# Kernel tuning notes

Measured on AMD Instinct MI355X. Metric: run time of the kernel, lower is better.

The kernel has to match this reference:

```python
import jax, jax.numpy as jnp
import numpy as np

N = 250000   # num nodes
E = 250000   # num edges (tree: ~one parent per node)
D = 128      # embed_size
H = 256      # MLP hidden
HOPS = 3


def _mlp(x, w1, b1, w2, b2):
    # Sequential(Linear, ReLU, Linear, ReLU, Dropout(eval=identity))
    return jax.nn.relu(jnp.dot(jax.nn.relu(jnp.dot(x, w1) + b1), w2) + b2)


def _scatter_mean(src, idx, n):
    s = jax.ops.segment_sum(src, idx, num_segments=n)
    c = jax.ops.segment_sum(jnp.ones((src.shape[0],), src.dtype), idx, num_segments=n)
    return s / jnp.maximum(c, 1.0)[:, None]


def setup_inputs() -> dict:
    key = jax.random.key(0)
    ks = jax.random.split(key, 32)
    u = lambda k, shp: jax.random.uniform(k, shp, jnp.float32, -0.1, 0.1)
    inp = {
        "batch_token": jax.random.normal(ks[0], (N, D), jnp.float32),
        "self_idx_batch": jax.random.randint(ks[1], (E,), 0, N),
        "parent_idx_batch": jax.random.randint(ks[2], (E,), 0, N),
        "root_mask": (jax.random.uniform(ks[3], (N,)) < 0.01).astype(jnp.float32),
        "leaf_mask": (jax.random.uniform(ks[4], (N,)) < 0.3).astype(jnp.float32),
        "start_token": jax.random.normal(ks[5], (D,), jnp.float32),
        "end_token": jax.random.normal(ks[6], (D,), jnp.float32),
        # MLP_V: D -> H -> D
        "Vw1": u(ks[7], (D, H)), "Vb1": u(ks[8], (H,)), "Vw2": u(ks[9], (H, D)), "Vb2": u(ks[10], (D,)),
        # MLP_E: 1 -> H -> D
        "Ew1": u(ks[11], (1, H)), "Eb1": u(ks[12], (H,)), "Ew2": u(ks[13], (H, D)), "Eb2": u(ks[14], (D,)),
        # MLP_p: 3D -> H -> D
        "Pw1": u(ks[15], (3 * D, H)), "Pb1": u(ks[16], (H,)), "Pw2": u(ks[17], (H, D)), "Pb2": u(ks[18], (D,)),
        # MLP_c: 3D -> H -> D
        "Cw1": u(ks[19], (3 * D, H)), "Cb1": u(ks[20], (H,)), "Cw2": u(ks[21], (H, D)), "Cb2": u(ks[22], (D,)),
        # MLP_aggr: 3D -> H -> D
        "Aw1": u(ks[23], (3 * D, H)), "Ab1": u(ks[24], (H,)), "Aw2": u(ks[25], (H, D)), "Ab2": u(ks[26], (D,)),
    }
    return inp


def reference(batch_token, self_idx_batch, parent_idx_batch, root_mask, leaf_mask,
              start_token, end_token,
              Vw1, Vb1, Vw2, Vb2,
              Ew1, Eb1, Ew2, Eb2,
              Pw1, Pb1, Pw2, Pb2,
              Cw1, Cb1, Cw2, Cb2,
              Aw1, Ab1, Aw2, Ab2):
    n = batch_token.shape[0]
    edge_in = _mlp(jnp.ones((1, 1), batch_token.dtype), Ew1, Eb1, Ew2, Eb2)   # [1,D]
    edge_out = _mlp(jnp.zeros((1, 1), batch_token.dtype), Ew1, Eb1, Ew2, Eb2)  # [1,D]
    e = self_idx_batch.shape[0]
    edge_in = jnp.broadcast_to(edge_in, (e, edge_in.shape[1]))
    edge_out = jnp.broadcast_to(edge_out, (e, edge_out.shape[1]))

    hidden = _mlp(batch_token, Vw1, Vb1, Vw2, Vb2)  # [N,D]
    for _ in range(HOPS):
        node_self = hidden[self_idx_batch]      # [E,D] gather
        node_parent = hidden[parent_idx_batch]  # [E,D] gather
        inp_parent = jnp.concatenate([node_parent, node_self, edge_out], axis=-1)  # [E,3D]
        inp_child = jnp.concatenate([node_self, node_parent, edge_in], axis=-1)    # [E,3D]
        S_p = _mlp(inp_parent, Pw1, Pb1, Pw2, Pb2)
        S_c = _mlp(inp_child, Cw1, Cb1, Cw2, Cb2)
        S_p = _scatter_mean(S_p, self_idx_batch, n)
        S_c = _scatter_mean(S_c, parent_idx_batch, n)
        S_p = S_p + root_mask[:, None] * start_token
        S_c = S_c + leaf_mask[:, None] * end_token
        x_aggr = jnp.concatenate([hidden, S_p, S_c], axis=-1)  # [N,3D]
        hidden = hidden + _mlp(x_aggr, Aw1, Ab1, Aw2, Ab2)
    return hidden
```

## Files before the change

### kernel.cpp

```cpp
#include <hip/hip_runtime.h>

typedef __attribute__((ext_vector_type(8))) short short8;
typedef __attribute__((ext_vector_type(4))) float f32x4;

#define DD 128
#define HH 256

__device__ __forceinline__ unsigned short f2bf(float f) {
  unsigned int u = __float_as_uint(f);
  u += 0x7fffu + ((u >> 16) & 1u);
  return (unsigned short)(u >> 16);
}
__device__ __forceinline__ float bf2f(unsigned short s) {
  return __uint_as_float(((unsigned int)s) << 16);
}
__device__ __forceinline__ f32x4 mfma16(short8 a, short8 b, f32x4 c) {
  return __builtin_amdgcn_mfma_f32_16x16x32_bf16(a, b, c, 0, 0, 0);
}

__global__ void wconv_all(const float* __restrict__ s0, const float* __restrict__ s1,
                          const float* __restrict__ s2, const float* __restrict__ s3,
                          const float* __restrict__ s4, const float* __restrict__ s5,
                          const float* __restrict__ s6, const float* __restrict__ s7,
                          unsigned short* __restrict__ d0, unsigned short* __restrict__ d1,
                          unsigned short* __restrict__ d2, unsigned short* __restrict__ d3,
                          unsigned short* __restrict__ d4, unsigned short* __restrict__ d5,
                          unsigned short* __restrict__ d6, unsigned short* __restrict__ d7) {
  int id = blockIdx.x * 256 + threadIdx.x;
  const float* src; unsigned short* dst; int K, Nout, kswap = 0, base;
  if (id < 32768)       { src = s0; dst = d0; K = 128; Nout = 256; base = 0; }
  else if (id < 65536)  { src = s1; dst = d1; K = 256; Nout = 128; base = 32768; }
  else if (id < 131072) { src = s2; dst = d2; K = 256; Nout = 256; base = 65536; kswap = 128; }
  else if (id < 163840) { src = s3; dst = d3; K = 256; Nout = 128; base = 131072; }
  else if (id < 229376) { src = s4; dst = d4; K = 256; Nout = 256; base = 163840; }
  else if (id < 262144) { src = s5; dst = d5; K = 256; Nout = 128; base = 229376; }
  else if (id < 360448) { src = s6; dst = d6; K = 384; Nout = 256; base = 262144; }
  else if (id < 393216) { src = s7; dst = d7; K = 256; Nout = 128; base = 360448; }
  else return;
  int lid = id - base;
  int n = lid / K, k = lid - n * K;
  int ks = k + kswap; if (ks >= K) ks -= K;
  dst[n * K + k] = f2bf(src[(size_t)ks * Nout + n]);
}

__global__ void prep_bias(const float* __restrict__ Ew1, const float* __restrict__ Eb1,
                          const float* __restrict__ Ew2, const float* __restrict__ Eb2,
                          const float* __restrict__ Pw1, const float* __restrict__ Pb1,
                          const float* __restrict__ Cw1, const float* __restrict__ Cb1,
                          float* __restrict__ b1P, float* __restrict__ b1C) {
  __shared__ float h1[HH], h0[HH], ein[DD], eout[DD];
  int t = threadIdx.x;
  h1[t] = fmaxf(Ew1[t] + Eb1[t], 0.f);
  h0[t] = fmaxf(Eb1[t], 0.f);
  __syncthreads();
  if (t < DD) {
    float s1 = Eb2[t], s0 = Eb2[t];
    for (int j = 0; j < HH; ++j) { s1 += h1[j] * Ew2[j * DD + t]; s0 += h0[j] * Ew2[j * DD + t]; }
    ein[t]  = fmaxf(s1, 0.f);
    eout[t] = fmaxf(s0, 0.f);
  }
  __syncthreads();
  float bp = Pb1[t], bc = Cb1[t];
  for (int d = 0; d < DD; ++d) {
    bp += eout[d] * Pw1[(size_t)(256 + d) * HH + t];
    bc += ein[d]  * Cw1[(size_t)(256 + d) * HH + t];
  }
  b1P[t] = bp; b1C[t] = bc;
}

__global__ void count_k(const int* __restrict__ selfI, const int* __restrict__ parI,
                        int* degP, int* degC, int E) {
  int id = blockIdx.x * 256 + threadIdx.x;
  if (id < E) { atomicAdd(&degP[selfI[id]], 1); atomicAdd(&degC[parI[id]], 1); }
}

__global__ void scan1_2(const int* __restrict__ srcA, int* __restrict__ dstA, int* __restrict__ partA,
                        const int* __restrict__ srcB, int* __restrict__ dstB, int* __restrict__ partB,
                        int n) {
  const int* src = blockIdx.y ? srcB : srcA;
  int* dst = blockIdx.y ? dstB : dstA;
  int* part = blockIdx.y ? partB : partA;
  __shared__ int sh[256];
  int t = threadIdx.x;
  int base = blockIdx.x * 1024 + t * 4;
  int v0 = base + 0 < n ? src[base + 0] : 0;
  int v1 = base + 1 < n ? src[base + 1] : 0;
  int v2 = base + 2 < n ? src[base + 2] : 0;
  int v3 = base + 3 < n ? src[base + 3] : 0;
  int tsum = v0 + v1 + v2 + v3;
  sh[t] = tsum;
  __syncthreads();
  for (int off = 1; off < 256; off <<= 1) {
    int y = (t >= off) ? sh[t - off] : 0;
    __syncthreads();
    if (t >= off) sh[t] += y;
    __syncthreads();
  }
  int ex = sh[t] - tsum;
  if (base + 0 < n) dst[base + 0] = ex;
  if (base + 1 < n) dst[base + 1] = ex + v0;
  if (base + 2 < n) dst[base + 2] = ex + v0 + v1;
  if (base + 3 < n) dst[base + 3] = ex + v0 + v1 + v2;
  if (t == 255) part[blockIdx.x] = sh[255];
}

__global__ void scan2_2(int* __restrict__ partA, int* __restrict__ partB, int m) {
  int* part = blockIdx.x ? partB : partA;
  __shared__ int sh[256];
  int t = threadIdx.x;
  int carry = 0;
  for (int base = 0; base < m; base += 256) {
    int v = (base + t < m) ? part[base + t] : 0;
    sh[t] = v;
    __syncthreads();
    for (int off = 1; off < 256; off <<= 1) {
      int y = (t >= off) ? sh[t - off] : 0;
      __syncthreads();
      if (t >= off) sh[t] += y;
      __syncthreads();
    }
    if (base + t < m) part[base + t] = carry + sh[t] - v;
    int tot = sh[255];
    __syncthreads();
    carry += tot;
  }
}

__global__ void scan3copy(int* __restrict__ offP, const int* __restrict__ partA, int* __restrict__ curP,
                          int* __restrict__ offC, const int* __restrict__ partB, int* __restrict__ curC,
                          int n) {
  int i = blockIdx.x * 256 + threadIdx.x;
  if (i < n) {
    int a = offP[i] + partA[i >> 10];
    int b = offC[i] + partB[i >> 10];
    offP[i] = a; curP[i] = a;
    offC[i] = b; curC[i] = b;
  }
}

__global__ void pos_k(const int* __restrict__ selfI, const int* __restrict__ parI,
                      int* curP, int* curC, int* posP, int* posC, int E) {
  int e = blockIdx.x * 256 + threadIdx.x;
  if (e < E) {
    posP[e] = atomicAdd(&curP[selfI[e]], 1);
    posC[e] = atomicAdd(&curC[parI[e]], 1);
  }
}

__global__ void reorder_k(const int* __restrict__ selfI, const int* __restrict__ parI,
                          const int* __restrict__ posP, const int* __restrict__ posC,
                          int* __restrict__ selfS, int* __restrict__ parS,
                          int* __restrict__ posCS, int E) {
  int e = blockIdx.x * 256 + threadIdx.x;
  if (e < E) {
    int slot = posP[e];
    selfS[slot] = selfI[e];
    parS[slot] = parI[e];
    posCS[slot] = posC[e];
  }
}

__global__ __launch_bounds__(512, 4) void v_kernel(
    const float* __restrict__ x, const unsigned short* __restrict__ W1t,
    const unsigned short* __restrict__ W2t, const float* __restrict__ b1,
    const float* __restrict__ b2, float* __restrict__ hidden,
    unsigned short* __restrict__ hbf, int n) {
  __shared__ __align__(16) unsigned short A[64 * 136];
  __shared__ __align__(16) unsigned short O1[64 * 264];
  int t = threadIdx.x;
  int w = t >> 6, lane = t & 63, ln = lane & 15, quad = lane >> 4, qo = quad * 8;
  long tile0 = (long)blockIdx.x * 64;
  int rl = t >> 3, part = t & 7;
  int c0 = part * 16;
  long gr = tile0 + rl;
  const float* src = x + (size_t)(gr < n ? gr : 0) * DD + c0;
  unsigned short* arow = A + rl * 136 + c0;
#pragma unroll
  for (int i = 0; i < 4; ++i) {
    float4 v = *(const float4*)(src + i * 4);
    *(ushort4*)(arow + i * 4) = make_ushort4(f2bf(v.x), f2bf(v.y), f2bf(v.z), f2bf(v.w));
  }
  __syncthreads();
  f32x4 acc[4][2];
#pragma unroll
  for (int m = 0; m < 4; ++m) {
    acc[m][0] = {0.f, 0.f, 0.f, 0.f}; acc[m][1] = {0.f, 0.f, 0.f, 0.f};
  }
#pragma unroll
  for (int kt = 0; kt < 4; ++kt) {
    short8 a[4];
#pragma unroll
    for (int m = 0; m < 4; ++m)
      a[m] = *(const short8*)(A + (m * 16 + ln) * 136 + kt * 32 + qo);
#pragma unroll
    for (int nn = 0; nn < 2; ++nn) {
      short8 b = *(const short8*)(W1t + (size_t)(w * 32 + nn * 16 + ln) * 128 + kt * 32 + qo);
#pragma unroll
      for (int m = 0; m < 4; ++m) acc[m][nn] = mfma16(a[m], b, acc[m][nn]);
    }
  }
#pragma unroll
  for (int nn = 0; nn < 2; ++nn) {
    int col = w * 32 + nn * 16 + ln;
    float bb = b1[col];
#pragma unroll
    for (int m = 0; m < 4; ++m)
#pragma unroll
      for (int r = 0; r < 4; ++r)
        O1[(m * 16 + quad * 4 + r) * 264 + col] = f2bf(fmaxf(acc[m][nn][r] + bb, 0.f));
  }
  __syncthreads();
  f32x4 acc2[4];
#pragma unroll
  for (int m = 0; m < 4; ++m) acc2[m] = {0.f, 0.f, 0.f, 0.f};
#pragma unroll
  for (int kt = 0; kt < 8; ++kt) {
    short8 b = *(const short8*)(W2t + (size_t)(w * 16 + ln) * 256 + kt * 32 + qo);
#pragma unroll
    for (int m = 0; m < 4; ++m) {
      short8 a = *(const short8*)(O1 + (m * 16 + ln) * 264 + kt * 32 + qo);
      acc2[m] = mfma16(a, b, acc2[m]);
    }
  }
  {
    int col = w * 16 + ln;
    float bb = b2[col];
#pragma unroll
    for (int m = 0; m < 4; ++m)
#pragma unroll
      for (int r = 0; r < 4; ++r) {
        long gr2 = tile0 + m * 16 + quad * 4 + r;
        if (gr2 < n) {
          float v = fmaxf(acc2[m][r] + bb, 0.f);
          hidden[gr2 * DD + col] = v;
          if (hbf) hbf[gr2 * DD + col] = f2bf(v);
        }
      }
  }
}

__global__ __launch_bounds__(512, 4) void edge_kernel(
    const float* __restrict__ hidden, const unsigned short* __restrict__ hbf,
    const int* __restrict__ selfS, const int* __restrict__ parS,
    const int* __restrict__ posCS,
    const unsigned short* __restrict__ Pw1t, const unsigned short* __restrict__ Pw2t,
    const unsigned short* __restrict__ Cw1t, const unsigned short* __restrict__ Cw2t,
    const float* __restrict__ b1P, const float* __restrict__ b1C,
    const float* __restrict__ b2P, const float* __restrict__ b2C,
    unsigned short* __restrict__ SpE, unsigned short* __restrict__ ScE, int E) {
  __shared__ __align__(16) unsigned short A[64 * 264];
  __shared__ __align__(16) unsigned short O1[64 * 264];
  int t = threadIdx.x;
  int w = t >> 6, lane = t & 63, ln = lane & 15, quad = lane >> 4, qo = quad * 8;
  long tile0 = (long)blockIdx.x * 64;
  int rl = t >> 3, part = t & 7;
  long ge = tile0 + rl;
  bool vrow = ge < E;
  int si = vrow ? selfS[ge] : 0;
  int pi = vrow ? parS[ge] : 0;
  unsigned short* dstA = A + rl * 264 + part * 32;
  if (hbf) {
    const unsigned short* srcb = (part < 4) ? (hbf + (size_t)si * DD + part * 32)
                                            : (hbf + (size_t)pi * DD + (part - 4) * 32);
#pragma unroll
    for (int i = 0; i < 4; ++i)
      *(short8*)(dstA + i * 8) = *(const short8*)(srcb + i * 8);
  } else {
    const float* src = (part < 4) ? (hidden + (size_t)si * DD + part * 32)
                                  : (hidden + (size_t)pi * DD + (part - 4) * 32);
#pragma unroll
    for (int i = 0; i < 8; ++i) {
      float4 v = *(const float4*)(src + i * 4);
      *(ushort4*)(dstA + i * 4) = make_ushort4(f2bf(v.x), f2bf(v.y), f2bf(v.z), f2bf(v.w));
    }
  }
  __syncthreads();

  f32x4 accP[4][2], accC[4][2];
#pragma unroll
  for (int m = 0; m < 4; ++m) {
    accP[m][0] = {0.f, 0.f, 0.f, 0.f}; accP[m][1] = {0.f, 0.f, 0.f, 0.f};
    accC[m][0] = {0.f, 0.f, 0.f, 0.f}; accC[m][1] = {0.f, 0.f, 0.f, 0.f};
  }
#pragma unroll
  for (int kt = 0; kt < 8; ++kt) {
    short8 a[4];
#pragma unroll
    for (int m = 0; m < 4; ++m)
      a[m] = *(const short8*)(A + (m * 16 + ln) * 264 + kt * 32 + qo);
#pragma unroll
    for (int nn = 0; nn < 2; ++nn) {
      short8 bp = *(const short8*)(Pw1t + (size_t)(w * 32 + nn * 16 + ln) * 256 + kt * 32 + qo);
      short8 bc = *(const short8*)(Cw1t + (size_t)(w * 32 + nn * 16 + ln) * 256 + kt * 32 + qo);
#pragma unroll
      for (int m = 0; m < 4; ++m) {
        accP[m][nn] = mfma16(a[m], bp, accP[m][nn]);
        accC[m][nn] = mfma16(a[m], bc, accC[m][nn]);
      }
    }
  }

#pragma unroll
  for (int mlp = 0; mlp < 2; ++mlp) {
    const unsigned short* W2t = mlp ? Cw2t : Pw2t;
    const float* b1 = mlp ? b1C : b1P;
    const float* b2 = mlp ? b2C : b2P;
    unsigned short* Sout = mlp ? ScE : SpE;
#pragma unroll
    for (int nn = 0; nn < 2; ++nn) {
      int col = w * 32 + nn * 16 + ln;
      float bb = b1[col];
#pragma unroll
      for (int m = 0; m < 4; ++m)
#pragma unroll
        for (int r = 0; r < 4; ++r) {
          float v = mlp ? accC[m][nn][r] : accP[m][nn][r];
          O1[(m * 16 + quad * 4 + r) * 264 + col] = f2bf(fmaxf(v + bb, 0.f));
        }
    }
    __syncthreads();
    f32x4 acc2[4];
#pragma unroll
    for (int m = 0; m < 4; ++m) acc2[m] = {0.f, 0.f, 0.f, 0.f};
#pragma unroll
    for (int kt = 0; kt < 8; ++kt) {
      short8 b = *(const short8*)(W2t + (size_t)(w * 16 + ln) * 256 + kt * 32 + qo);
#pragma unroll
      for (int m = 0; m < 4; ++m) {
        short8 a = *(const short8*)(O1 + (m * 16 + ln) * 264 + kt * 32 + qo);
        acc2[m] = mfma16(a, b, acc2[m]);
      }
    }
    __syncthreads();
    {
      int col = w * 16 + ln;
      float bb = b2[col];
#pragma unroll
      for (int m = 0; m < 4; ++m)
#pragma unroll
        for (int r = 0; r < 4; ++r)
          O1[(m * 16 + quad * 4 + r) * 264 + col] = f2bf(fmaxf(acc2[m][r] + bb, 0.f));
    }
    __syncthreads();
    if (vrow) {
      size_t dpos = mlp ? (size_t)posCS[ge] : (size_t)ge;
      const unsigned short* srow = O1 + rl * 264 + part * 16;
      ushort4* dst = (ushort4*)(Sout + dpos * DD + part * 16);
#pragma unroll
      for (int i = 0; i < 4; ++i) dst[i] = *(const ushort4*)(srow + i * 4);
    }
    __syncthreads();
  }
}

__global__ __launch_bounds__(512, 4) void node_kernel(
    float* __restrict__ hidden, unsigned short* __restrict__ hbf,
    const unsigned short* __restrict__ SpE, const unsigned short* __restrict__ ScE,
    const int* __restrict__ offP, const int* __restrict__ degP,
    const int* __restrict__ offC, const int* __restrict__ degC,
    const float* __restrict__ rootM, const float* __restrict__ leafM,
    const float* __restrict__ startT, const float* __restrict__ endT,
    const unsigned short* __restrict__ W1t, const unsigned short* __restrict__ W2t,
    const float* __restrict__ b1, const float* __restrict__ b2, int n) {
  __shared__ __align__(16) unsigned short A[64 * 392];
  int t = threadIdx.x;
  int w = t >> 6, lane = t & 63, ln = lane & 15, quad = lane >> 4, qo = quad * 8;
  long tile0 = (long)blockIdx.x * 64;
  int rl = t >> 3, part = t & 7;
  int c0 = part * 16;
  long gr = tile0 + rl;
  long g = (gr < n) ? gr : 0;
  unsigned short* arow = A + rl * 392;
  if (hbf) {
    const unsigned short* hrowb = hbf + (size_t)g * DD + c0;
    *(short8*)(arow + c0)     = *(const short8*)(hrowb);
    *(short8*)(arow + c0 + 8) = *(const short8*)(hrowb + 8);
  } else {
    const float* hrow = hidden + (size_t)g * DD + c0;
#pragma unroll
    for (int i = 0; i < 4; ++i) {
      float4 h = *(const float4*)(hrow + i * 4);
      *(ushort4*)(arow + c0 + i * 4) = make_ushort4(f2bf(h.x), f2bf(h.y), f2bf(h.z), f2bf(h.w));
    }
  }
  {
    int off = offP[g], dg = degP[g];
    float s[16];
#pragma unroll
    for (int i = 0; i < 16; ++i) s[i] = 0.f;
    for (int j = 0; j < dg; ++j) {
      const unsigned short* rr = SpE + (size_t)(off + j) * DD + c0;
#pragma unroll
      for (int i = 0; i < 4; ++i) {
        ushort4 u = *(const ushort4*)(rr + i * 4);
        s[i * 4 + 0] += bf2f(u.x); s[i * 4 + 1] += bf2f(u.y);
        s[i * 4 + 2] += bf2f(u.z); s[i * 4 + 3] += bf2f(u.w);
      }
    }
    float ip = 1.f / fmaxf((float)dg, 1.f);
    float rm = rootM[g];
#pragma unroll
    for (int i = 0; i < 4; ++i) {
      float4 st = *(const float4*)(startT + c0 + i * 4);
      *(ushort4*)(arow + 128 + c0 + i * 4) = make_ushort4(
          f2bf(s[i * 4 + 0] * ip + rm * st.x), f2bf(s[i * 4 + 1] * ip + rm * st.y),
          f2bf(s[i * 4 + 2] * ip + rm * st.z), f2bf(s[i * 4 + 3] * ip + rm * st.w));
    }
  }
  {
    int off = offC[g], dg = degC[g];
    float s[16];
#pragma unroll
    for (int i = 0; i < 16; ++i) s[i] = 0.f;
    for (int j = 0; j < dg; ++j) {
      const unsigned short* rr = ScE + (size_t)(off + j) * DD + c0;
#pragma unroll
      for (int i = 0; i < 4; ++i) {
        ushort4 u = *(const ushort4*)(rr + i * 4);
        s[i * 4 + 0] += bf2f(u.x); s[i * 4 + 1] += bf2f(u.y);
        s[i * 4 + 2] += bf2f(u.z); s[i * 4 + 3] += bf2f(u.w);
      }
    }
    float ic = 1.f / fmaxf((float)dg, 1.f);
    float lm = leafM[g];
#pragma unroll
    for (int i = 0; i < 4; ++i) {
      float4 et = *(const float4*)(endT + c0 + i * 4);
      *(ushort4*)(arow + 256 + c0 + i * 4) = make_ushort4(
          f2bf(s[i * 4 + 0] * ic + lm * et.x), f2bf(s[i * 4 + 1] * ic + lm * et.y),
          f2bf(s[i * 4 + 2] * ic + lm * et.z), f2bf(s[i * 4 + 3] * ic + lm * et.w));
    }
  }
  __syncthreads();
  f32x4 acc[4][2];
#pragma unroll
  for (int m = 0; m < 4; ++m) {
    acc[m][0] = {0.f, 0.f, 0.f, 0.f}; acc[m][1] = {0.f, 0.f, 0.f, 0.f};
  }
#pragma unroll
  for (int kt = 0; kt < 12; ++kt) {
    short8 a[4];
#pragma unroll
    for (int m = 0; m < 4; ++m)
      a[m] = *(const short8*)(A + (m * 16 + ln) * 392 + kt * 32 + qo);
#pragma unroll
    for (int nn = 0; nn < 2; ++nn) {
      short8 b = *(const short8*)(W1t + (size_t)(w * 32 + nn * 16 + ln) * 384 + kt * 32 + qo);
#pragma unroll
      for (int m = 0; m < 4; ++m) acc[m][nn] = mfma16(a[m], b, acc[m][nn]);
    }
  }
  __syncthreads();
#pragma unroll
  for (int nn = 0; nn < 2; ++nn) {
    int col = w * 32 + nn * 16 + ln;
    float bb = b1[col];
#pragma unroll
    for (int m = 0; m < 4; ++m)
#pragma unroll
      for (int r = 0; r < 4; ++r)
        A[(m * 16 + quad * 4 + r) * 392 + col] = f2bf(fmaxf(acc[m][nn][r] + bb, 0.f));
  }
  __syncthreads();
  f32x4 acc2[4];
#pragma unroll
  for (int m = 0; m < 4; ++m) acc2[m] = {0.f, 0.f, 0.f, 0.f};
#pragma unroll
  for (int kt = 0; kt < 8; ++kt) {
    short8 b = *(const short8*)(W2t + (size_t)(w * 16 + ln) * 256 + kt * 32 + qo);
#pragma unroll
    for (int m = 0; m < 4; ++m) {
      short8 a = *(const short8*)(A + (m * 16 + ln) * 392 + kt * 32 + qo);
      acc2[m] = mfma16(a, b, acc2[m]);
    }
  }
  __syncthreads();
  {
    int col = w * 16 + ln;
    float bb = b2[col];
#pragma unroll
    for (int m = 0; m < 4; ++m)
#pragma unroll
      for (int r = 0; r < 4; ++r)
        ((float*)(A + (size_t)(m * 16 + quad * 4 + r) * 392))[col] =
            fmaxf(acc2[m][r] + bb, 0.f);
  }
  __syncthreads();
  if (gr < n) {
    const float* F = (const float*)(A + (size_t)rl * 392);
    float* hrow = hidden + (size_t)gr * DD + c0;
    unsigned short* brow = hbf ? hbf + (size_t)gr * DD + c0 : nullptr;
#pragma unroll
    for (int i = 0; i < 4; ++i) {
      float4 v = *(const float4*)(F + c0 + i * 4);
      float4 h = *(const float4*)(hrow + i * 4);
      h.x += v.x; h.y += v.y; h.z += v.z; h.w += v.w;
      *(float4*)(hrow + i * 4) = h;
      if (brow)
        *(ushort4*)(brow + i * 4) = make_ushort4(f2bf(h.x), f2bf(h.y), f2bf(h.z), f2bf(h.w));
    }
  }
}

extern "C" void kernel_launch(void* const* d_in, const int* in_sizes, int n_in,
                              void* d_out, int out_size, void* d_ws, size_t ws_size,
                              hipStream_t stream) {
  const float* batch  = (const float*)d_in[0];
  const int*   selfI  = (const int*)d_in[1];
  const int*   parI   = (const int*)d_in[2];
  const float* rootM  = (const float*)d_in[3];
  const float* leafM  = (const float*)d_in[4];
  const float* startT = (const float*)d_in[5];
  const float* endT   = (const float*)d_in[6];
  const float* Vw1 = (const float*)d_in[7],  *Vb1 = (const float*)d_in[8];
  const float* Vw2 = (const float*)d_in[9],  *Vb2 = (const float*)d_in[10];
  const float* Ew1 = (const float*)d_in[11], *Eb1 = (const float*)d_in[12];
  const float* Ew2 = (const float*)d_in[13], *Eb2 = (const float*)d_in[14];
  const float* Pw1 = (const float*)d_in[15], *Pb1 = (const float*)d_in[16];
  const float* Pw2 = (const float*)d_in[17], *Pb2 = (const float*)d_in[18];
  const float* Cw1 = (const float*)d_in[19], *Cb1 = (const float*)d_in[20];
  const float* Cw2 = (const float*)d_in[21], *Cb2 = (const float*)d_in[22];
  const float* Aw1 = (const float*)d_in[23], *Ab1 = (const float*)d_in[24];
  const float* Aw2 = (const float*)d_in[25], *Ab2 = (const float*)d_in[26];

  const int N = in_sizes[3];
  const int E = in_sizes[1];
  float* out = (float*)d_out;

  char* p = (char*)d_ws;
  auto nxt = [&](size_t sz) { char* r = p; p += (sz + 255) & ~(size_t)255; return r; };
  unsigned short* SpE = (unsigned short*)nxt((size_t)E * DD * 2);
  unsigned short* ScE = (unsigned short*)nxt((size_t)E * DD * 2);
  int* degP = (int*)nxt((size_t)N * 4);
  int* degC = (int*)nxt((size_t)N * 4);
  int* offP = (int*)nxt((size_t)N * 4);
  int* offC = (int*)nxt((size_t)N * 4);
  int* curP = (int*)nxt((size_t)N * 4);
  int* curC = (int*)nxt((size_t)N * 4);
  int* posP = (int*)nxt((size_t)E * 4);
  int* posC = (int*)nxt((size_t)E * 4);
  int* selfS = (int*)nxt((size_t)E * 4);
  int* parS = (int*)nxt((size_t)E * 4);
  int* posCS = (int*)nxt((size_t)E * 4);
  int* partA = (int*)nxt(4096);
  int* partB = (int*)nxt(4096);
  unsigned short* Vw1t = (unsigned short*)nxt((size_t)128 * 256 * 2);
  unsigned short* Vw2t = (unsigned short*)nxt((size_t)256 * 128 * 2);
  unsigned short* Pw1t = (unsigned short*)nxt((size_t)256 * 256 * 2);
  unsigned short* Pw2t = (unsigned short*)nxt((size_t)256 * 128 * 2);
  unsigned short* Cw1t = (unsigned short*)nxt((size_t)256 * 256 * 2);
  unsigned short* Cw2t = (unsigned short*)nxt((size_t)256 * 128 * 2);
  unsigned short* Aw1t = (unsigned short*)nxt((size_t)384 * 256 * 2);
  unsigned short* Aw2t = (unsigned short*)nxt((size_t)256 * 128 * 2);
  float* b1P = (float*)nxt(256 * 4);
  float* b1C = (float*)nxt(256 * 4);
  unsigned short* Hbf = (unsigned short*)nxt((size_t)N * DD * 2);
  if ((size_t)(p - (char*)d_ws) > ws_size) Hbf = nullptr;

  hipMemsetAsync(degP, 0, (size_t)N * 4, stream);
  hipMemsetAsync(degC, 0, (size_t)N * 4, stream);

  auto blk = [](int total) { return dim3((total + 255) / 256); };
  wconv_all<<<blk(393216), 256, 0, stream>>>(Vw1, Vw2, Pw1, Pw2, Cw1, Cw2, Aw1, Aw2,
                                             Vw1t, Vw2t, Pw1t, Pw2t, Cw1t, Cw2t, Aw1t, Aw2t);

  prep_bias<<<1, 256, 0, stream>>>(Ew1, Eb1, Ew2, Eb2, Pw1, Pb1, Cw1, Cb1, b1P, b1C);
  count_k<<<blk(E), 256, 0, stream>>>(selfI, parI, degP, degC, E);

  int NB = (N + 1023) / 1024;
  scan1_2<<<dim3(NB, 2), 256, 0, stream>>>(degP, offP, partA, degC, offC, partB, N);
  scan2_2<<<2, 256, 0, stream>>>(partA, partB, NB);
  scan3copy<<<blk(N), 256, 0, stream>>>(offP, partA, curP, offC, partB, curC, N);
  pos_k<<<blk(E), 256, 0, stream>>>(selfI, parI, curP, curC, posP, posC, E);
  reorder_k<<<blk(E), 256, 0, stream>>>(selfI, parI, posP, posC, selfS, parS, posCS, E);

  dim3 gN((N + 63) / 64), gE((E + 63) / 64);
  v_kernel<<<gN, 512, 0, stream>>>(batch, Vw1t, Vw2t, Vb1, Vb2, out, Hbf, N);

  for (int hop = 0; hop < 3; ++hop) {
    edge_kernel<<<gE, 512, 0, stream>>>(out, Hbf, selfS, parS, posCS,
                                        Pw1t, Pw2t, Cw1t, Cw2t, b1P, b1C, Pb2, Cb2,
                                        SpE, ScE, E);
    node_kernel<<<gN, 512, 0, stream>>>(out, Hbf, SpE, ScE, offP, degP, offC, degC,
                                        rootM, leafM, startT, endT,
                                        Aw1t, Aw2t, Ab1, Ab2, N);
  }
}
```

Baseline: 1.841 ms.

## Make edge kernel persistent with prefetched gathers; merge node segment reductions

The edge kernel becomes a persistent grid-stride loop capped at 512 blocks. Each iteration prefetches the next tile's indices and gathered hidden rows into registers while the current tile's MLP runs, with biases hoisted out of the loop. The node kernel now reads fp32 hidden once into registers (removing a second read at the residual), interleaves the parent and child segment-sum loops with wider loads, and skips the bf16 hidden copy on the last hop. The aim is to hide gather latency and cut redundant memory traffic, at the cost of higher register pressure and fewer resident blocks.

```diff
diff --git a/kernel.cpp b/kernel.cpp
--- a/kernel.cpp
+++ b/kernel.cpp
@@ -16,6 +16,33 @@
 }
 __device__ __forceinline__ f32x4 mfma16(short8 a, short8 b, f32x4 c) {
   return __builtin_amdgcn_mfma_f32_16x16x32_bf16(a, b, c, 0, 0, 0);
+}
+__device__ __forceinline__ short8 cvt8(float4 a, float4 b) {
+  union { ushort4 u[2]; short8 s; } x;
+  x.u[0] = make_ushort4(f2bf(a.x), f2bf(a.y), f2bf(a.z), f2bf(a.w));
+  x.u[1] = make_ushort4(f2bf(b.x), f2bf(b.y), f2bf(b.z), f2bf(b.w));
+  return x.s;
+}
+
+__device__ __forceinline__ void gather_row(
+    const unsigned short* hbf, const float* hidden, int si, int pi, int part,
+    short8& g0, short8& g1, short8& g2, short8& g3) {
+  if (hbf) {
+    const unsigned short* s = (part < 4) ? hbf + (size_t)si * DD + part * 32
+                                         : hbf + (size_t)pi * DD + (part - 4) * 32;
+    g0 = *(const short8*)(s);
+    g1 = *(const short8*)(s + 8);
+    g2 = *(const short8*)(s + 16);
+    g3 = *(const short8*)(s + 24);
+  } else {
+    const float* s = (part < 4) ? hidden + (size_t)si * DD + part * 32
+                                : hidden + (size_t)pi * DD + (part - 4) * 32;
+    float4 a, b;
+    a = *(const float4*)(s);      b = *(const float4*)(s + 4);  g0 = cvt8(a, b);
+    a = *(const float4*)(s + 8);  b = *(const float4*)(s + 12); g1 = cvt8(a, b);
+    a = *(const float4*)(s + 16); b = *(const float4*)(s + 20); g2 = cvt8(a, b);
+    a = *(const float4*)(s + 24); b = *(const float4*)(s + 28); g3 = cvt8(a, b);
+  }
 }
 
 __global__ void wconv_all(const float* __restrict__ s0, const float* __restrict__ s1,
@@ -247,84 +274,87 @@
     const unsigned short* __restrict__ Cw1t, const unsigned short* __restrict__ Cw2t,
     const float* __restrict__ b1P, const float* __restrict__ b1C,
     const float* __restrict__ b2P, const float* __restrict__ b2C,
-    unsigned short* __restrict__ SpE, unsigned short* __restrict__ ScE, int E) {
+    unsigned short* __restrict__ SpE, unsigned short* __restrict__ ScE,
+    int E, int ntiles) {
   __shared__ __align__(16) unsigned short A[64 * 264];
   __shared__ __align__(16) unsigned short O1[64 * 264];
   int t = threadIdx.x;
   int w = t >> 6, lane = t & 63, ln = lane & 15, quad = lane >> 4, qo = quad * 8;
-  long tile0 = (long)blockIdx.x * 64;
   int rl = t >> 3, part = t & 7;
-  long ge = tile0 + rl;
-  bool vrow = ge < E;
+  unsigned short* dstA = A + rl * 264 + part * 32;
+
+  float bbP0 = b1P[w * 32 + ln], bbP1 = b1P[w * 32 + 16 + ln];
+  float bbC0 = b1C[w * 32 + ln], bbC1 = b1C[w * 32 + 16 + ln];
+  float b2Pr = b2P[w * 16 + ln], b2Cr = b2C[w * 16 + ln];
+
+  int tile = blockIdx.x;
+  long ge = (long)tile * 64 + rl;
+  bool vrow = (tile < ntiles) && (ge < E);
   int si = vrow ? selfS[ge] : 0;
   int pi = vrow ? parS[ge] : 0;
-  unsigned short* dstA = A + rl * 264 + part * 32;
-  if (hbf) {
-    const unsigned short* srcb = (part < 4) ? (hbf + (size_t)si * DD + part * 32)
-                                            : (hbf + (size_t)pi * DD + (part - 4) * 32);
-#pragma unroll
-    for (int i = 0; i < 4; ++i)
-      *(short8*)(dstA + i * 8) = *(const short8*)(srcb + i * 8);
-  } else {
-    const float* src = (part < 4) ? (hidden + (size_t)si * DD + part * 32)
-                                  : (hidden + (size_t)pi * DD + (part - 4) * 32);
-#pragma unroll
-    for (int i = 0; i < 8; ++i) {
-      float4 v = *(const float4*)(src + i * 4);
-      *(ushort4*)(dstA + i * 4) = make_ushort4(f2bf(v.x), f2bf(v.y), f2bf(v.z), f2bf(v.w));
-    }
-  }
-  __syncthreads();
-
-  f32x4 accP[4][2], accC[4][2];
-#pragma unroll
-  for (int m = 0; m < 4; ++m) {
-    accP[m][0] = {0.f, 0.f, 0.f, 0.f}; accP[m][1] = {0.f, 0.f, 0.f, 0.f};
-    accC[m][0] = {0.f, 0.f, 0.f, 0.f}; accC[m][1] = {0.f, 0.f, 0.f, 0.f};
-  }
-#pragma unroll
-  for (int kt = 0; kt < 8; ++kt) {
-    short8 a[4];
-#pragma unroll
-    for (int m = 0; m < 4; ++m)
-      a[m] = *(const short8*)(A + (m * 16 + ln) * 264 + kt * 32 + qo);
-#pragma unroll
-    for (int nn = 0; nn < 2; ++nn) {
-      short8 bp = *(const short8*)(Pw1t + (size_t)(w * 32 + nn * 16 + ln) * 256 + kt * 32 + qo);
-      short8 bc = *(const short8*)(Cw1t + (size_t)(w * 32 + nn * 16 + ln) * 256 + kt * 32 + qo);
-#pragma unroll
-      for (int m = 0; m < 4; ++m) {
-        accP[m][nn] = mfma16(a[m], bp, accP[m][nn]);
-        accC[m][nn] = mfma16(a[m], bc, accC[m][nn]);
+  int dpc = vrow ? posCS[ge] : 0;
+  short8 g0, g1, g2, g3;
+  gather_row(hbf, hidden, si, pi, part, g0, g1, g2, g3);
+
+  while (tile < ntiles) {
+    *(short8*)(dstA) = g0;
+    *(short8*)(dstA + 8) = g1;
+    *(short8*)(dstA + 16) = g2;
+    *(short8*)(dstA + 24) = g3;
+    __syncthreads();
+
+    int ntile = tile + (int)gridDim.x;
+    long ge2 = (long)ntile * 64 + rl;
+    bool vrow2 = (ntile < ntiles) && (ge2 < E);
+    int si2 = vrow2 ? selfS[ge2] : 0;
+    int pi2 = vrow2 ? parS[ge2] : 0;
+    int dpc2 = vrow2 ? posCS[ge2] : 0;
+
+    f32x4 accP[4][2], accC[4][2];
+#pragma unroll
+    for (int m = 0; m < 4; ++m) {
+      accP[m][0] = {0.f, 0.f, 0.f, 0.f}; accP[m][1] = {0.f, 0.f, 0.f, 0.f};
+      accC[m][0] = {0.f, 0.f, 0.f, 0.f}; accC[m][1] = {0.f, 0.f, 0.f, 0.f};
+    }
+#pragma unroll
+    for (int kt = 0; kt < 8; ++kt) {
+      short8 a[4];
+#pragma unroll
+      for (int m = 0; m < 4; ++m)
+        a[m] = *(const short8*)(A + (m * 16 + ln) * 264 + kt * 32 + qo);
+#pragma unroll
+      for (int nn = 0; nn < 2; ++nn) {
+        short8 bp = *(const short8*)(Pw1t + (size_t)(w * 32 + nn * 16 + ln) * 256 + kt * 32 + qo);
+        short8 bc = *(const short8*)(Cw1t + (size_t)(w * 32 + nn * 16 + ln) * 256 + kt * 32 + qo);
+#pragma unroll
+        for (int m = 0; m < 4; ++m) {
+          accP[m][nn] = mfma16(a[m], bp, accP[m][nn]);
+          accC[m][nn] = mfma16(a[m], bc, accC[m][nn]);
+        }
       }
     }
-  }
-
-#pragma unroll
-  for (int mlp = 0; mlp < 2; ++mlp) {
-    const unsigned short* W2t = mlp ? Cw2t : Pw2t;
-    const float* b1 = mlp ? b1C : b1P;
-    const float* b2 = mlp ? b2C : b2P;
-    unsigned short* Sout = mlp ? ScE : SpE;
+
 #pragma unroll
     for (int nn = 0; nn < 2; ++nn) {
       int col = w * 32 + nn * 16 + ln;
-      float bb = b1[col];
+      float bb = nn ? bbP1 : bbP0;
 #pragma unroll
       for (int m = 0; m < 4; ++m)
 #pragma unroll
-        for (int r = 0; r < 4; ++r) {
-          float v = mlp ? accC[m][nn][r] : accP[m][nn][r];
-          O1[(m * 16 + quad * 4 + r) * 264 + col] = f2bf(fmaxf(v + bb, 0.f));
-        }
-    }
-    __syncthreads();
+        for (int r = 0; r < 4; ++r)
+          O1[(m * 16 + quad * 4 + r) * 264 + col] = f2bf(fmaxf(accP[m][nn][r] + bb, 0.f));
+    }
+    __syncthreads();
+
+    short8 n0, n1, n2, n3;
+    gather_row(hbf, hidden, si2, pi2, part, n0, n1, n2, n3);
+
     f32x4 acc2[4];
 #pragma unroll
     for (int m = 0; m < 4; ++m) acc2[m] = {0.f, 0.f, 0.f, 0.f};
 #pragma unroll
     for (int kt = 0; kt < 8; ++kt) {
-      short8 b = *(const short8*)(W2t + (size_t)(w * 16 + ln) * 256 + kt * 32 + qo);
+      short8 b = *(const short8*)(Pw2t + (size_t)(w * 16 + ln) * 256 + kt * 32 + qo);
 #pragma unroll
       for (int m = 0; m < 4; ++m) {
         short8 a = *(const short8*)(O1 + (m * 16 + ln) * 264 + kt * 32 + qo);
@@ -334,22 +364,61 @@
     __syncthreads();
     {
       int col = w * 16 + ln;
-      float bb = b2[col];
 #pragma unroll
       for (int m = 0; m < 4; ++m)
 #pragma unroll
         for (int r = 0; r < 4; ++r)
-          O1[(m * 16 + quad * 4 + r) * 264 + col] = f2bf(fmaxf(acc2[m][r] + bb, 0.f));
+          O1[(m * 16 + quad * 4 + r) * 264 + col] = f2bf(fmaxf(acc2[m][r] + b2Pr, 0.f));
     }
     __syncthreads();
     if (vrow) {
-      size_t dpos = mlp ? (size_t)posCS[ge] : (size_t)ge;
       const unsigned short* srow = O1 + rl * 264 + part * 16;
-      ushort4* dst = (ushort4*)(Sout + dpos * DD + part * 16);
+      ushort4* dst = (ushort4*)(SpE + (size_t)ge * DD + part * 16);
 #pragma unroll
       for (int i = 0; i < 4; ++i) dst[i] = *(const ushort4*)(srow + i * 4);
     }
     __syncthreads();
+
+#pragma unroll
+    for (int nn = 0; nn < 2; ++nn) {
+      int col = w * 32 + nn * 16 + ln;
+      float bb = nn ? bbC1 : bbC0;
+#pragma unroll
+      for (int m = 0; m < 4; ++m)
+#pragma unroll
+        for (int r = 0; r < 4; ++r)
+          O1[(m * 16 + quad * 4 + r) * 264 + col] = f2bf(fmaxf(accC[m][nn][r] + bb, 0.f));
+    }
+    __syncthreads();
+#pragma unroll
+    for (int m = 0; m < 4; ++m) acc2[m] = {0.f, 0.f, 0.f, 0.f};
+#pragma unroll
+    for (int kt = 0; kt < 8; ++kt) {
+      short8 b = *(const short8*)(Cw2t + (size_t)(w * 16 + ln) * 256 + kt * 32 + qo);
+#pragma unroll
+      for (int m = 0; m < 4; ++m) {
+        short8 a = *(const short8*)(O1 + (m * 16 + ln) * 264 + kt * 32 + qo);
+        acc2[m] = mfma16(a, b, acc2[m]);
+      }
+    }
+    __syncthreads();
+    {
+      int col = w * 16 + ln;
+#pragma unroll
+      for (int m = 0; m < 4; ++m)
+#pragma unroll
+        for (int r = 0; r < 4; ++r)
+          O1[(m * 16 + quad * 4 + r) * 264 + col] = f2bf(fmaxf(acc2[m][r] + b2Cr, 0.f));
+    }
+    __syncthreads();
+    if (vrow) {
+      const unsigned short* srow = O1 + rl * 264 + part * 16;
+      ushort4* dst = (ushort4*)(ScE + (size_t)dpc * DD + part * 16);
+#pragma unroll
+      for (int i = 0; i < 4; ++i) dst[i] = *(const ushort4*)(srow + i * 4);
+    }
+    tile = ntile; vrow = vrow2; ge = ge2; dpc = dpc2;
+    g0 = n0; g1 = n1; g2 = n2; g3 = n3;
   }
 }
 
@@ -370,65 +439,65 @@
   int c0 = part * 16;
   long gr = tile0 + rl;
   long g = (gr < n) ? gr : 0;
+  const float* hrow = hidden + (size_t)g * DD + c0;
+  float4 h0 = *(const float4*)(hrow);
+  float4 h1 = *(const float4*)(hrow + 4);
+  float4 h2 = *(const float4*)(hrow + 8);
+  float4 h3 = *(const float4*)(hrow + 12);
+  int offp = offP[g], dgp = degP[g];
+  int offc = offC[g], dgc = degC[g];
+  float rm = rootM[g], lm = leafM[g];
+
   unsigned short* arow = A + rl * 392;
-  if (hbf) {
-    const unsigned short* hrowb = hbf + (size_t)g * DD + c0;
-    *(short8*)(arow + c0)     = *(const short8*)(hrowb);
-    *(short8*)(arow + c0 + 8) = *(const short8*)(hrowb + 8);
-  } else {
-    const float* hrow = hidden + (size_t)g * DD + c0;
-#pragma unroll
-    for (int i = 0; i < 4; ++i) {
-      float4 h = *(const float4*)(hrow + i * 4);
-      *(ushort4*)(arow + c0 + i * 4) = make_ushort4(f2bf(h.x), f2bf(h.y), f2bf(h.z), f2bf(h.w));
+  *(ushort4*)(arow + c0)      = make_ushort4(f2bf(h0.x), f2bf(h0.y), f2bf(h0.z), f2bf(h0.w));
+  *(ushort4*)(arow + c0 + 4)  = make_ushort4(f2bf(h1.x), f2bf(h1.y), f2bf(h1.z), f2bf(h1.w));
+  *(ushort4*)(arow + c0 + 8)  = make_ushort4(f2bf(h2.x), f2bf(h2.y), f2bf(h2.z), f2bf(h2.w));
+  *(ushort4*)(arow + c0 + 12) = make_ushort4(f2bf(h3.x), f2bf(h3.y), f2bf(h3.z), f2bf(h3.w));
+
+  float sp[16], sc[16];
+#pragma unroll
+  for (int i = 0; i < 16; ++i) { sp[i] = 0.f; sc[i] = 0.f; }
+  const unsigned short* rp = SpE + (size_t)offp * DD + c0;
+  const unsigned short* rc = ScE + (size_t)offc * DD + c0;
+  int jm = dgp > dgc ? dgp : dgc;
+  for (int j = 0; j < jm; ++j) {
+    if (j < dgp) {
+      short8 u0 = *(const short8*)(rp);
+      short8 u1 = *(const short8*)(rp + 8);
+#pragma unroll
+      for (int k = 0; k < 8; ++k) {
+        sp[k]     += bf2f((unsigned short)u0[k]);
+        sp[8 + k] += bf2f((unsigned short)u1[k]);
+      }
+      rp += DD;
+    }
+    if (j < dgc) {
+      short8 u0 = *(const short8*)(rc);
+      short8 u1 = *(const short8*)(rc + 8);
+#pragma unroll
+      for (int k = 0; k < 8; ++k) {
+        sc[k]     += bf2f((unsigned short)u0[k]);
+        sc[8 + k] += bf2f((unsigned short)u1[k]);
+      }
+      rc += DD;
     }
   }
   {
-    int off = offP[g], dg = degP[g];
-    float s[16];
-#pragma unroll
-    for (int i = 0; i < 16; ++i) s[i] = 0.f;
-    for (int j = 0; j < dg; ++j) {
-      const unsigned short* rr = SpE + (size_t)(off + j) * DD + c0;
-#pragma unroll
-      for (int i = 0; i < 4; ++i) {
-        ushort4 u = *(const ushort4*)(rr + i * 4);
-        s[i * 4 + 0] += bf2f(u.x); s[i * 4 + 1] += bf2f(u.y);
-        s[i * 4 + 2] += bf2f(u.z); s[i * 4 + 3] += bf2f(u.w);
-      }
-    }
-    float ip = 1.f / fmaxf((float)dg, 1.f);
-    float rm = rootM[g];
+    float ip = 1.f / fmaxf((float)dgp, 1.f);
 #pragma unroll
     for (int i = 0; i < 4; ++i) {
       float4 st = *(const float4*)(startT + c0 + i * 4);
       *(ushort4*)(arow + 128 + c0 + i * 4) = make_ushort4(
-          f2bf(s[i * 4 + 0] * ip + rm * st.x), f2bf(s[i * 4 + 1] * ip + rm * st.y),
-          f2bf(s[i * 4 + 2] * ip + rm * st.z), f2bf(s[i * 4 + 3] * ip + rm * st.w));
-    }
-  }
-  {
-    int off = offC[g], dg = degC[g];
-    float s[16];
-#pragma unroll
-    for (int i = 0; i < 16; ++i) s[i] = 0.f;
-    for (int j = 0; j < dg; ++j) {
-      const unsigned short* rr = ScE + (size_t)(off + j) * DD + c0;
-#pragma unroll
-      for (int i = 0; i < 4; ++i) {
-        ushort4 u = *(const ushort4*)(rr + i * 4);
-        s[i * 4 + 0] += bf2f(u.x); s[i * 4 + 1] += bf2f(u.y);
-        s[i * 4 + 2] += bf2f(u.z); s[i * 4 + 3] += bf2f(u.w);
-      }
-    }
-    float ic = 1.f / fmaxf((float)dg, 1.f);
-    float lm = leafM[g];
+          f2bf(sp[i * 4 + 0] * ip + rm * st.x), f2bf(sp[i * 4 + 1] * ip + rm * st.y),
+          f2bf(sp[i * 4 + 2] * ip + rm * st.z), f2bf(sp[i * 4 + 3] * ip + rm * st.w));
+    }
+    float ic = 1.f / fmaxf((float)dgc, 1.f);
 #pragma unroll
     for (int i = 0; i < 4; ++i) {
       float4 et = *(const float4*)(endT + c0 + i * 4);
       *(ushort4*)(arow + 256 + c0 + i * 4) = make_ushort4(
-          f2bf(s[i * 4 + 0] * ic + lm * et.x), f2bf(s[i * 4 + 1] * ic + lm * et.y),
-          f2bf(s[i * 4 + 2] * ic + lm * et.z), f2bf(s[i * 4 + 3] * ic + lm * et.w));
+          f2bf(sc[i * 4 + 0] * ic + lm * et.x), f2bf(sc[i * 4 + 1] * ic + lm * et.y),
+          f2bf(sc[i * 4 + 2] * ic + lm * et.z), f2bf(sc[i * 4 + 3] * ic + lm * et.w));
     }
   }
   __syncthreads();
@@ -487,17 +556,26 @@
   }
   __syncthreads();
   if (gr < n) {
-    const float* F = (const float*)(A + (size_t)rl * 392);
-    float* hrow = hidden + (size_t)gr * DD + c0;
+    const float* F = (const float*)(A + (size_t)rl * 392) + c0;
+    float* hout = hidden + (size_t)gr * DD + c0;
     unsigned short* brow = hbf ? hbf + (size_t)gr * DD + c0 : nullptr;
-#pragma unroll
-    for (int i = 0; i < 4; ++i) {
-      float4 v = *(const float4*)(F + c0 + i * 4);
-      float4 h = *(const float4*)(hrow + i * 4);
-      h.x += v.x; h.y += v.y; h.z += v.z; h.w += v.w;
-      *(float4*)(hrow + i * 4) = h;
-      if (brow)
-        *(ushort4*)(brow + i * 4) = make_ushort4(f2bf(h.x), f2bf(h.y), f2bf(h.z), f2bf(h.w));
+    float4 v0 = *(const float4*)(F);
+    float4 v1 = *(const float4*)(F + 4);
+    float4 v2 = *(const float4*)(F + 8);
+    float4 v3 = *(const float4*)(F + 12);
+    h0.x += v0.x; h0.y += v0.y; h0.z += v0.z; h0.w += v0.w;
+    h1.x += v1.x; h1.y += v1.y; h1.z += v1.z; h1.w += v1.w;
+    h2.x += v2.x; h2.y += v2.y; h2.z += v2.z; h2.w += v2.w;
+    h3.x += v3.x; h3.y += v3.y; h3.z += v3.z; h3.w += v3.w;
+    *(float4*)(hout) = h0;
+    *(float4*)(hout + 4) = h1;
+    *(float4*)(hout + 8) = h2;
+    *(float4*)(hout + 12) = h3;
+    if (brow) {
+      *(ushort4*)(brow)     = make_ushort4(f2bf(h0.x), f2bf(h0.y), f2bf(h0.z), f2bf(h0.w));
+      *(ushort4*)(brow + 4) = make_ushort4(f2bf(h1.x), f2bf(h1.y), f2bf(h1.z), f2bf(h1.w));
+      *(ushort4*)(brow + 8) = make_ushort4(f2bf(h2.x), f2bf(h2.y), f2bf(h2.z), f2bf(h2.w));
+      *(ushort4*)(brow + 12) = make_ushort4(f2bf(h3.x), f2bf(h3.y), f2bf(h3.z), f2bf(h3.w));
     }
   }
 }
@@ -574,14 +652,17 @@
   pos_k<<<blk(E), 256, 0, stream>>>(selfI, parI, curP, curC, posP, posC, E);
   reorder_k<<<blk(E), 256, 0, stream>>>(selfI, parI, posP, posC, selfS, parS, posCS, E);
 
-  dim3 gN((N + 63) / 64), gE((E + 63) / 64);
+  dim3 gN((N + 63) / 64);
+  int ET = (E + 63) / 64;
+  int gEp = ET < 512 ? ET : 512;
   v_kernel<<<gN, 512, 0, stream>>>(batch, Vw1t, Vw2t, Vb1, Vb2, out, Hbf, N);
 
   for (int hop = 0; hop < 3; ++hop) {
-    edge_kernel<<<gE, 512, 0, stream>>>(out, Hbf, selfS, parS, posCS,
-                                        Pw1t, Pw2t, Cw1t, Cw2t, b1P, b1C, Pb2, Cb2,
-                                        SpE, ScE, E);
-    node_kernel<<<gN, 512, 0, stream>>>(out, Hbf, SpE, ScE, offP, degP, offC, degC,
+    edge_kernel<<<gEp, 512, 0, stream>>>(out, Hbf, selfS, parS, posCS,
+                                         Pw1t, Pw2t, Cw1t, Cw2t, b1P, b1C, Pb2, Cb2,
+                                         SpE, ScE, E, ET);
+    node_kernel<<<gN, 512, 0, stream>>>(out, (hop < 2) ? Hbf : (unsigned short*)nullptr,
+                                        SpE, ScE, offP, degP, offC, degC,
                                         rootM, leafM, startT, endT,
                                         Aw1t, Aw2t, Ab1, Ab2, N);
   }
```

Measured after the change: 2.340 ms. 27.1% more time.
